# Optimization experiments

Hardware: AMD Instinct MI355X
Metric: run time of the kernel (lower is better)

Reference implementation:

```python
import jax, jax.numpy as jnp
import numpy as np
import math

B, S, D, H, L, V = 16, 512, 1024, 16, 128, 32000
DH = D // H


def _posenc(s, d):
    pos = np.arange(s, dtype=np.float32)[:, None]
    div = np.exp(np.arange(0, d, 2, dtype=np.float32) * (-math.log(10000.0) / d))
    pe = np.zeros((s, d), dtype=np.float32)
    pe[:, 0::2] = np.sin(pos * div)
    pe[:, 1::2] = np.cos(pos * div)
    return jnp.asarray(pe)


def _ln(x, g, b):
    m = jnp.mean(x, axis=-1, keepdims=True)
    v = jnp.mean((x - m) ** 2, axis=-1, keepdims=True)
    return (x - m) / jnp.sqrt(v + 1e-5) * g + b


def setup_inputs():
    key = jax.random.key(0)
    ks = jax.random.split(key, 16)
    w = lambda k, *sh: 0.02 * jax.random.normal(k, sh, dtype=jnp.float32)
    return {
        'x': jax.random.randint(ks[0], (B, S), 0, V),
        'embed': w(ks[1], V, D),
        'Wq': w(ks[2], D, D), 'bq': jnp.zeros((D,), jnp.float32),
        'Wk': w(ks[3], D, D), 'bk': jnp.zeros((D,), jnp.float32),
        'Wv': w(ks[4], D, D), 'bv': jnp.zeros((D,), jnp.float32),
        'Wo': w(ks[5], D, D), 'bo': jnp.zeros((D,), jnp.float32),
        'g1': jnp.ones((D,), jnp.float32), 'be1': jnp.zeros((D,), jnp.float32),
        'W1': w(ks[6], D, D), 'bf1': jnp.zeros((D,), jnp.float32),
        'W2': w(ks[7], D, D), 'bf2': jnp.zeros((D,), jnp.float32),
        'g2': jnp.ones((D,), jnp.float32), 'be2': jnp.zeros((D,), jnp.float32),
        'g3': jnp.ones((D,), jnp.float32), 'be3': jnp.zeros((D,), jnp.float32),
        'Wmu': w(ks[8], D, L), 'bmu': jnp.zeros((L,), jnp.float32),
        'Wsig': w(ks[9], D, L), 'bsig': jnp.zeros((L,), jnp.float32),
        'eps': jax.random.normal(ks[10], (B, S, L), dtype=jnp.float32),
    }


def reference(x, embed, Wq, bq, Wk, bk, Wv, bv, Wo, bo, g1, be1, W1, bf1, W2, bf2,
              g2, be2, g3, be3, Wmu, bmu, Wsig, bsig, eps):
    h = embed[x] * jnp.asarray(D ** 0.5, jnp.float32)          # [B,S,D]
    h = h + _posenc(S, D)                                       # dropout = identity (eval)
    h = _ln(h, g1, be1)
    # attention (faithful to source: raw reshape head-split, scale = dh/2)
    Q = (h @ Wq + bq).reshape(B, H, S, DH)
    K = (h @ Wk + bk).reshape(B, H, S, DH)
    Vv = (h @ Wv + bv).reshape(B, H, S, DH)
    scores = jnp.einsum('bhqd,bhkd->bhqk', Q, K) / (DH / 2.0)
    attn = jax.nn.softmax(scores, axis=-1)
    ctx = jnp.einsum('bhqk,bhkd->bhqd', attn, Vv).reshape(B, S, D)
    ctx = ctx @ Wo + bo
    h = h + ctx
    h = _ln(h, g2, be2)
    f = jax.nn.leaky_relu(h @ W1 + bf1, 0.01) @ W2 + bf2
    h = f + f                                                    # source: x = ffn(x); x = x + drop2(x)
    h = _ln(h, g3, be3)
    mu = h @ Wmu + bmu
    sigma = jnp.exp(h @ Wsig + bsig)
    z = mu + sigma * eps
    return z
```

## Files before the change

### kernel.cpp

```cpp
#include <hip/hip_runtime.h>
#include <cstdint>


typedef __bf16 bf16;
typedef __bf16 bf16x8 __attribute__((ext_vector_type(8)));
typedef __bf16 bf16x4 __attribute__((ext_vector_type(4)));
typedef float f32x4 __attribute__((ext_vector_type(4)));

#define MFMA16(a, b, c) __builtin_amdgcn_mfma_f32_16x16x32_bf16((a), (b), (c), 0, 0, 0)

#if __has_builtin(__builtin_amdgcn_exp2f)
#define EXP2F(x) __builtin_amdgcn_exp2f(x)
#else
#define EXP2F(x) exp2f(x)
#endif

__device__ __forceinline__ void async16(const bf16* g, bf16* l) {
  __builtin_amdgcn_global_load_lds(
      (const __attribute__((address_space(1))) unsigned int*)g,
      (__attribute__((address_space(3))) unsigned int*)l, 16, 0, 0);
}

struct TP8 {
  const float* src[8];
  bf16* dst[8];
  int ncol[8];
};
__global__ __launch_bounds__(256) void transpose8_kernel(TP8 p) {
  const int z = blockIdx.z;
  const int N = p.ncol[z];
  const int tk = blockIdx.x * 64, tn = blockIdx.y * 64;
  if (tn >= N) return;
  const float* __restrict__ W = p.src[z];
  bf16* __restrict__ Wt = p.dst[z];
  __shared__ float tile[64][65];
  const int a = threadIdx.x >> 6, b = threadIdx.x & 63;
#pragma unroll
  for (int i = 0; i < 16; ++i) {
    int k = a + i * 4;
    tile[k][b] = W[(size_t)(tk + k) * N + tn + b];
  }
  __syncthreads();
#pragma unroll
  for (int i = 0; i < 16; ++i) {
    int n = a + i * 4;
    Wt[(size_t)(tn + n) * 1024 + tk + b] = (bf16)tile[b][n];
  }
}

__global__ __launch_bounds__(256) void embed_ln_kernel(const int* __restrict__ x,
                                                       const float* __restrict__ emb,
                                                       const float* __restrict__ g,
                                                       const float* __restrict__ be,
                                                       bf16* __restrict__ obf) {
  const int w = threadIdx.x >> 6, lane = threadIdx.x & 63;
  const int row = blockIdx.x * 4 + w;
  const int s = row & 511;
  const int t = x[row];
  const int c0 = lane * 16;
  const float* er = emb + (size_t)t * 1024 + c0;
  float o[16];
#pragma unroll
  for (int i = 0; i < 4; ++i) {
    const float4 e = *(const float4*)(er + i * 4);
    o[i * 4 + 0] = e.x; o[i * 4 + 1] = e.y; o[i * 4 + 2] = e.z; o[i * 4 + 3] = e.w;
  }
#pragma unroll
  for (int p = 0; p < 8; ++p) {
    const int cc = c0 + 2 * p;
    const float freq = __expf((float)cc * (-9.210340371976184f / 1024.0f));
    const float ang = (float)s * freq;
    o[2 * p] = o[2 * p] * 32.0f + __sinf(ang);
    o[2 * p + 1] = o[2 * p + 1] * 32.0f + __cosf(ang);
  }
  float sm = 0.f, q = 0.f;
#pragma unroll
  for (int j = 0; j < 16; ++j) { sm += o[j]; q += o[j] * o[j]; }
#pragma unroll
  for (int off = 1; off < 64; off <<= 1) {
    sm += __shfl_xor(sm, off);
    q += __shfl_xor(q, off);
  }
  const float mean = sm * (1.0f / 1024.0f);
  const float var = q * (1.0f / 1024.0f) - mean * mean;
  const float rstd = rsqrtf(var + 1e-5f);
  bf16 ob[16];
#pragma unroll
  for (int i = 0; i < 4; ++i) {
    const float4 gv = *(const float4*)(g + c0 + i * 4);
    const float4 bv = *(const float4*)(be + c0 + i * 4);
    const float gvv[4] = {gv.x, gv.y, gv.z, gv.w};
    const float bvv[4] = {bv.x, bv.y, bv.z, bv.w};
#pragma unroll
    for (int j = 0; j < 4; ++j)
      ob[i * 4 + j] = (bf16)((o[i * 4 + j] - mean) * rstd * gvv[j] + bvv[j]);
  }
  bf16* dst = obf + (size_t)row * 1024 + c0;
  *(uint4*)dst = *(const uint4*)&ob[0];
  *(uint4*)(dst + 8) = *(const uint4*)&ob[8];
}

__global__ __launch_bounds__(256) void ln_kernel(const bf16* __restrict__ in,
                                                 const float* __restrict__ g,
                                                 const float* __restrict__ be,
                                                 bf16* __restrict__ obf) {
  const int w = threadIdx.x >> 6, lane = threadIdx.x & 63;
  const int row = blockIdx.x * 4 + w;
  const int c0 = lane * 16;
  const bf16* src = in + (size_t)row * 1024 + c0;
  const bf16x8 v0 = *(const bf16x8*)src;
  const bf16x8 v1 = *(const bf16x8*)(src + 8);
  float v[16];
#pragma unroll
  for (int j = 0; j < 8; ++j) { v[j] = (float)v0[j]; v[8 + j] = (float)v1[j]; }
  float s = 0.f, q = 0.f;
#pragma unroll
  for (int j = 0; j < 16; ++j) { s += v[j]; q += v[j] * v[j]; }
#pragma unroll
  for (int off = 1; off < 64; off <<= 1) {
    s += __shfl_xor(s, off);
    q += __shfl_xor(q, off);
  }
  const float mean = s * (1.0f / 1024.0f);
  const float var = q * (1.0f / 1024.0f) - mean * mean;
  const float rstd = rsqrtf(var + 1e-5f);
  bf16 ob[16];
#pragma unroll
  for (int i = 0; i < 4; ++i) {
    const float4 gv = *(const float4*)(g + c0 + i * 4);
    const float4 bv = *(const float4*)(be + c0 + i * 4);
    const float gvv[4] = {gv.x, gv.y, gv.z, gv.w};
    const float bvv[4] = {bv.x, bv.y, bv.z, bv.w};
#pragma unroll
    for (int j = 0; j < 4; ++j)
      ob[i * 4 + j] = (bf16)((v[i * 4 + j] - mean) * rstd * gvv[j] + bvv[j]);
  }
  bf16* dst = obf + (size_t)row * 1024 + c0;
  *(uint4*)dst = *(const uint4*)&ob[0];
  *(uint4*)(dst + 8) = *(const uint4*)&ob[8];
}

template <int MODE, int BK>
__global__ __launch_bounds__(256) void gemm_kernel(
    const bf16* __restrict__ A, const bf16* __restrict__ Bt,
    const float* __restrict__ b0f, const float* __restrict__ b1f,
    const float* __restrict__ b2f,
    bf16* __restrict__ o0, bf16* __restrict__ o1, bf16* __restrict__ o2,
    const bf16* __restrict__ residb,
    int M, int N, int K) {
  __shared__ __attribute__((aligned(16))) bf16 Asm[2][128 * BK];
  __shared__ __attribute__((aligned(16))) bf16 Bsm[2][128 * BK];
  constexpr int KH = BK / 32;
  constexpr int SPT = (128 * BK / 8) / 256;
  const int tid = threadIdx.x;
  const int wv = tid >> 6, lane = tid & 63;
  const int quad = lane >> 4, l15 = lane & 15;
  const int m0 = blockIdx.x * 128, n0 = blockIdx.y * 128;
  const int wm = wv & 1, wn = wv >> 1;

  f32x4 acc[4][4];
#pragma unroll
  for (int i = 0; i < 4; ++i)
#pragma unroll
    for (int j = 0; j < 4; ++j) acc[i][j] = {0.f, 0.f, 0.f, 0.f};

  const bf16* Aglb[SPT];
  const bf16* Bglb[SPT];
  int soff[SPT];
#pragma unroll
  for (int i = 0; i < SPT; ++i) {
    const int s = tid + i * 256;
    int row, col;
    if constexpr (BK == 32) {
      row = s >> 2;
      col = (s & 3) ^ ((row >> 1) & 3);
    } else {
      row = s >> 3;
      col = (s & 7) ^ (row & 7);
    }
    Aglb[i] = A + (size_t)(m0 + row) * K + col * 8;
    Bglb[i] = Bt + (size_t)(n0 + row) * K + col * 8;
    soff[i] = s * 8;
  }

#pragma unroll
  for (int i = 0; i < SPT; ++i) async16(Aglb[i], &Asm[0][soff[i]]);
#pragma unroll
  for (int i = 0; i < SPT; ++i) async16(Bglb[i], &Bsm[0][soff[i]]);
  __syncthreads();

  const int nk = K / BK;
  for (int k = 0; k < nk; ++k) {
    const int cur = k & 1, nxt = cur ^ 1;
    bf16x8 af[4][KH], bfr[4][KH];
#pragma unroll
    for (int mi = 0; mi < 4; ++mi) {
      const int row = wm * 64 + mi * 16 + l15;
#pragma unroll
      for (int h = 0; h < KH; ++h) {
        int pos;
        if constexpr (BK == 32) pos = quad ^ ((row >> 1) & 3);
        else pos = (h * 4 + quad) ^ (row & 7);
        af[mi][h] = *(const bf16x8*)(&Asm[cur][(row * (BK / 8) + pos) * 8]);
      }
    }
#pragma unroll
    for (int ni = 0; ni < 4; ++ni) {
      const int row = wn * 64 + ni * 16 + l15;
#pragma unroll
      for (int h = 0; h < KH; ++h) {
        int pos;
        if constexpr (BK == 32) pos = quad ^ ((row >> 1) & 3);
        else pos = (h * 4 + quad) ^ (row & 7);
        bfr[ni][h] = *(const bf16x8*)(&Bsm[cur][(row * (BK / 8) + pos) * 8]);
      }
    }
    if (k + 1 < nk) {
      const int ko = (k + 1) * BK;
#pragma unroll
      for (int i = 0; i < SPT; ++i) async16(Aglb[i] + ko, &Asm[nxt][soff[i]]);
#pragma unroll
      for (int i = 0; i < SPT; ++i) async16(Bglb[i] + ko, &Bsm[nxt][soff[i]]);
    }
#pragma unroll
    for (int h = 0; h < KH; ++h)
#pragma unroll
      for (int mi = 0; mi < 4; ++mi)
#pragma unroll
        for (int ni = 0; ni < 4; ++ni)
          acc[mi][ni] = MFMA16(af[mi][h], bfr[ni][h], acc[mi][ni]);
    __syncthreads();
  }

  const int part = (MODE == 6) ? (blockIdx.y >> 3) : 0;
  bf16* ob = o0;
  const float* bp = b0f;
  if constexpr (MODE == 6) {
    ob = (part == 0) ? o0 : (part == 1 ? o1 : o2);
    bp = (part == 0) ? b0f : (part == 1 ? b1f : b2f);
  }
#pragma unroll
  for (int ni = 0; ni < 4; ++ni) {
    const int col = n0 + wn * 64 + ni * 16 + l15;
    const int cl = (MODE == 6) ? (col - part * 1024) : col;
    const float bv = bp[cl];
#pragma unroll
    for (int mi = 0; mi < 4; ++mi) {
#pragma unroll
      for (int r = 0; r < 4; ++r) {
        const int row = m0 + wm * 64 + mi * 16 + quad * 4 + r;
        float v = acc[mi][ni][r] + bv;
        if constexpr (MODE == 1) {
          const size_t idx = (size_t)row * N + col;
          o0[idx] = (bf16)(v + (float)residb[idx]);
        } else if constexpr (MODE == 2) {
          o0[(size_t)row * N + col] = (bf16)(v > 0.f ? v : 0.01f * v);
        } else if constexpr (MODE == 3) {
          o0[(size_t)row * N + col] = (bf16)(2.0f * v);
        } else {
          ob[(size_t)row * 1024 + cl] = (bf16)v;
        }
      }
    }
  }
}

__global__ __launch_bounds__(256) void gemm_musig(const bf16* __restrict__ A,
                                                  const bf16* __restrict__ Bt,
                                                  const float* __restrict__ bmu,
                                                  const float* __restrict__ bsig,
                                                  float* __restrict__ of) {
  constexpr int BK = 64;
  __shared__ __attribute__((aligned(16))) bf16 Asm[2][64 * BK];
  __shared__ __attribute__((aligned(16))) bf16 Bsm[2][128 * BK];
  const int tid = threadIdx.x;
  const int wv = tid >> 6, lane = tid & 63;
  const int quad = lane >> 4, l15 = lane & 15;
  const int m0 = blockIdx.x * 64, n0 = blockIdx.y * 128;
  const int wm = wv & 1, wn = wv >> 1;

  f32x4 acc[2][4];
#pragma unroll
  for (int i = 0; i < 2; ++i)
#pragma unroll
    for (int j = 0; j < 4; ++j) acc[i][j] = {0.f, 0.f, 0.f, 0.f};

  const bf16* Aglb[2];
  int asoff[2];
#pragma unroll
  for (int i = 0; i < 2; ++i) {
    const int s = tid + i * 256;
    const int row = s >> 3, col = (s & 7) ^ (row & 7);
    Aglb[i] = A + (size_t)(m0 + row) * 1024 + col * 8;
    asoff[i] = s * 8;
  }
  const bf16* Bglb[4];
  int bsoff[4];
#pragma unroll
  for (int i = 0; i < 4; ++i) {
    const int s = tid + i * 256;
    const int row = s >> 3, col = (s & 7) ^ (row & 7);
    Bglb[i] = Bt + (size_t)(n0 + row) * 1024 + col * 8;
    bsoff[i] = s * 8;
  }

#pragma unroll
  for (int i = 0; i < 2; ++i) async16(Aglb[i], &Asm[0][asoff[i]]);
#pragma unroll
  for (int i = 0; i < 4; ++i) async16(Bglb[i], &Bsm[0][bsoff[i]]);
  __syncthreads();

  for (int k = 0; k < 16; ++k) {
    const int cur = k & 1, nxt = cur ^ 1;
    bf16x8 af[2][2], bfr[4][2];
#pragma unroll
    for (int mi = 0; mi < 2; ++mi) {
      const int row = wm * 32 + mi * 16 + l15;
#pragma unroll
      for (int h = 0; h < 2; ++h) {
        const int pos = (h * 4 + quad) ^ (row & 7);
        af[mi][h] = *(const bf16x8*)(&Asm[cur][(row * 8 + pos) * 8]);
      }
    }
#pragma unroll
    for (int ni = 0; ni < 4; ++ni) {
      const int row = wn * 64 + ni * 16 + l15;
#pragma unroll
      for (int h = 0; h < 2; ++h) {
        const int pos = (h * 4 + quad) ^ (row & 7);
        bfr[ni][h] = *(const bf16x8*)(&Bsm[cur][(row * 8 + pos) * 8]);
      }
    }
    if (k + 1 < 16) {
      const int ko = (k + 1) * BK;
#pragma unroll
      for (int i = 0; i < 2; ++i) async16(Aglb[i] + ko, &Asm[nxt][asoff[i]]);
#pragma unroll
      for (int i = 0; i < 4; ++i) async16(Bglb[i] + ko, &Bsm[nxt][bsoff[i]]);
    }
#pragma unroll
    for (int h = 0; h < 2; ++h)
#pragma unroll
      for (int mi = 0; mi < 2; ++mi)
#pragma unroll
        for (int ni = 0; ni < 4; ++ni)
          acc[mi][ni] = MFMA16(af[mi][h], bfr[ni][h], acc[mi][ni]);
    __syncthreads();
  }

#pragma unroll
  for (int ni = 0; ni < 4; ++ni) {
    const int col = n0 + wn * 64 + ni * 16 + l15;
    const float bv = (col < 128) ? bmu[col] : bsig[col - 128];
#pragma unroll
    for (int mi = 0; mi < 2; ++mi) {
#pragma unroll
      for (int r = 0; r < 4; ++r) {
        const int row = m0 + wm * 32 + mi * 16 + quad * 4 + r;
        of[(size_t)row * 256 + col] = acc[mi][ni][r] + bv;
      }
    }
  }
}

__global__ __launch_bounds__(256) void vtrans_kernel(const bf16* __restrict__ Vb,
                                                     bf16* __restrict__ VtG) {
  __shared__ float t[64][65];
  const int bh = blockIdx.x, kt = blockIdx.y;
  const int tid = threadIdx.x;
  const bf16* src = Vb + (size_t)bh * 32768 + (size_t)kt * 4096;
#pragma unroll
  for (int i = 0; i < 2; ++i) {
    int s = i * 256 + tid;
    int r = s >> 3, c = (s & 7) * 8;
    bf16x8 v = *(const bf16x8*)(src + (size_t)s * 8);
#pragma unroll
    for (int j = 0; j < 8; ++j) t[r][c + j] = (float)v[j];
  }
  __syncthreads();
  bf16* dst = VtG + (size_t)bh * 32768 + kt * 64;
#pragma unroll
  for (int i = 0; i < 2; ++i) {
    int s = i * 256 + tid;
    int d = s >> 3, kc = (s & 7) * 8;
    bf16 tmp[8];
#pragma unroll
    for (int j = 0; j < 8; ++j) tmp[j] = (bf16)t[kc + j][d];
    *(uint4*)(dst + (size_t)d * 512 + kc) = *(const uint4*)tmp;
  }
}

__global__ __launch_bounds__(256) void attn_kernel(const bf16* __restrict__ Qg,
                                                   const bf16* __restrict__ Kg,
                                                   const bf16* __restrict__ Vt,
                                                   bf16* __restrict__ ctx) {
  __shared__ __attribute__((aligned(16))) bf16 Ksm[128 * 64];
  __shared__ __attribute__((aligned(16))) bf16 Vsm[64 * 128];
  __shared__ __attribute__((aligned(16))) bf16 Psm[4][16 * 128];
  const int tid = threadIdx.x;
  const int w = tid >> 6, lane = tid & 63;
  const int quad = lane >> 4, l15 = lane & 15;
  const int bh = blockIdx.x;
  const size_t base = (size_t)bh * 32768;
  const bf16* Vth = Vt + base;
  const int qbase = blockIdx.y * 128 + w * 32;
  const f32x4 fz = {0.f, 0.f, 0.f, 0.f};

  bf16x8 a[2][2];
#pragma unroll
  for (int qt = 0; qt < 2; ++qt)
#pragma unroll
    for (int hf = 0; hf < 2; ++hf) {
      bf16x8 tq = *(const bf16x8*)(Qg + base +
                   (size_t)(qbase + qt * 16 + l15) * 64 + hf * 32 + quad * 8);
#pragma unroll
      for (int e = 0; e < 8; ++e) tq[e] = (bf16)((float)tq[e] * 0.045111758f);
      a[qt][hf] = tq;
    }

  f32x4 o[2][4];
  float l_i[2][4];
#pragma unroll
  for (int qt = 0; qt < 2; ++qt)
#pragma unroll
    for (int i = 0; i < 4; ++i) { o[qt][i] = fz; l_i[qt][i] = 0.f; }

  for (int kv0 = 0; kv0 < 512; kv0 += 128) {
#pragma unroll
    for (int i = 0; i < 4; ++i) {
      int s = i * 256 + tid;
      int r = s >> 3, c = (s & 7) ^ (r & 7);
      async16(Kg + base + (size_t)(kv0 + r) * 64 + c * 8, &Ksm[s * 8]);
    }
#pragma unroll
    for (int i = 0; i < 4; ++i) {
      int s = i * 256 + tid;
      int d = s >> 4, cs = s & 15;
      int c = (cs & 8) | ((cs & 7) ^ (d & 7));
      async16(Vth + (size_t)d * 512 + kv0 + c * 8, &Vsm[s * 8]);
    }
    __syncthreads();

    f32x4 sc[2][8];
#pragma unroll
    for (int j = 0; j < 8; ++j) {
      const int n = j * 16 + l15;
      const bf16x8 k0 = *(const bf16x8*)(&Ksm[(n * 8 + (quad ^ (n & 7))) * 8]);
      const bf16x8 k1 = *(const bf16x8*)(&Ksm[(n * 8 + ((4 + quad) ^ (n & 7))) * 8]);
      sc[0][j] = MFMA16(a[0][0], k0, fz);
      sc[0][j] = MFMA16(a[0][1], k1, sc[0][j]);
      sc[1][j] = MFMA16(a[1][0], k0, fz);
      sc[1][j] = MFMA16(a[1][1], k1, sc[1][j]);
    }

    bf16* ps = &Psm[w][0];
#pragma unroll
    for (int qt = 0; qt < 2; ++qt) {
#pragma unroll
      for (int r = 0; r < 4; ++r) {
        const int prow = quad * 4 + r;
        float sum = 0.f;
#pragma unroll
        for (int j = 0; j < 8; ++j) {
          const float p = EXP2F(sc[qt][j][r]);
          sum += p;
          const int col = j * 16 + l15;
          const int cc = col >> 3;
          const int ccs = (cc & 8) | ((cc & 7) ^ (prow & 7));
          ps[prow * 128 + ccs * 8 + (col & 7)] = (bf16)p;
        }
        l_i[qt][r] += sum;
      }
#pragma unroll
      for (int c32 = 0; c32 < 4; ++c32) {
        const int pc = c32 * 4 + quad;
        const int pcs = (pc & 8) | ((pc & 7) ^ (l15 & 7));
        const bf16x8 pf = *(const bf16x8*)(ps + l15 * 128 + pcs * 8);
#pragma unroll
        for (int ni = 0; ni < 4; ++ni) {
          const int d = ni * 16 + l15;
          const int vcs = (pc & 8) | ((pc & 7) ^ (d & 7));
          const bf16x8 vf = *(const bf16x8*)(&Vsm[(d * 16 + vcs) * 8]);
          o[qt][ni] = MFMA16(pf, vf, o[qt][ni]);
        }
      }
    }
    __syncthreads();
  }

#pragma unroll
  for (int qt = 0; qt < 2; ++qt) {
#pragma unroll
    for (int r = 0; r < 4; ++r) {
      float l = l_i[qt][r];
      l += __shfl_xor(l, 1);
      l += __shfl_xor(l, 2);
      l += __shfl_xor(l, 4);
      l += __shfl_xor(l, 8);
      const float inv = 1.0f / l;
#pragma unroll
      for (int ni = 0; ni < 4; ++ni)
        ctx[base + (size_t)(qbase + qt * 16 + quad * 4 + r) * 64 + ni * 16 + l15]
            = (bf16)(o[qt][ni][r] * inv);
    }
  }
}

__global__ __launch_bounds__(256) void final_kernel(const float* __restrict__ musg,
                                                    const float* __restrict__ eps,
                                                    float* __restrict__ z) {
  const int i = blockIdx.x * 256 + threadIdx.x;
  const int row = i >> 5;
  const int c = (i & 31) * 4;
  const float4 m = *(const float4*)(musg + (size_t)row * 256 + c);
  const float4 s = *(const float4*)(musg + (size_t)row * 256 + 128 + c);
  const float4 e = *(const float4*)(eps + (size_t)row * 128 + c);
  float4 r;
  r.x = m.x + __expf(s.x) * e.x;
  r.y = m.y + __expf(s.y) * e.y;
  r.z = m.z + __expf(s.z) * e.z;
  r.w = m.w + __expf(s.w) * e.w;
  *(float4*)(z + (size_t)row * 128 + c) = r;
}

extern "C" void kernel_launch(void* const* d_in, const int* in_sizes, int n_in,
                              void* d_out, int out_size, void* d_ws, size_t ws_size,
                              hipStream_t stream) {
  (void)in_sizes; (void)n_in; (void)out_size; (void)ws_size;
  const int* x = (const int*)d_in[0];
  const float* emb = (const float*)d_in[1];
  const float* Wq = (const float*)d_in[2];
  const float* bq = (const float*)d_in[3];
  const float* Wk = (const float*)d_in[4];
  const float* bkb = (const float*)d_in[5];
  const float* Wv = (const float*)d_in[6];
  const float* bv = (const float*)d_in[7];
  const float* Wo = (const float*)d_in[8];
  const float* bo = (const float*)d_in[9];
  const float* g1 = (const float*)d_in[10];
  const float* be1 = (const float*)d_in[11];
  const float* W1 = (const float*)d_in[12];
  const float* bf1 = (const float*)d_in[13];
  const float* W2 = (const float*)d_in[14];
  const float* bf2 = (const float*)d_in[15];
  const float* g2 = (const float*)d_in[16];
  const float* be2 = (const float*)d_in[17];
  const float* g3 = (const float*)d_in[18];
  const float* be3 = (const float*)d_in[19];
  const float* Wmu = (const float*)d_in[20];
  const float* bmu = (const float*)d_in[21];
  const float* Wsig = (const float*)d_in[22];
  const float* bsig = (const float*)d_in[23];
  const float* eps = (const float*)d_in[24];
  float* z = (float*)d_out;

  const int M = 8192, D = 1024;
  char* ws = (char*)d_ws;
  size_t off = 0;
  auto alloc = [&](size_t b) {
    char* p = ws + off;
    off += (b + 255) & ~(size_t)255;
    return p;
  };
  bf16* wqkvT = (bf16*)alloc((size_t)3072 * 1024 * 2);
  bf16* woT = (bf16*)alloc((size_t)1024 * 1024 * 2);
  bf16* w1T = (bf16*)alloc((size_t)1024 * 1024 * 2);
  bf16* w2T = (bf16*)alloc((size_t)1024 * 1024 * 2);
  bf16* wmsT = (bf16*)alloc((size_t)256 * 1024 * 2);
  bf16* hb = (bf16*)alloc((size_t)M * D * 2);
  bf16* Qb = (bf16*)alloc((size_t)M * D * 2);
  bf16* Kb = (bf16*)alloc((size_t)M * D * 2);
  bf16* Vb = (bf16*)alloc((size_t)M * D * 2);
  bf16* VtG = (bf16*)alloc((size_t)M * D * 2);
  bf16* Cb = (bf16*)alloc((size_t)M * D * 2);
  bf16* h2b = (bf16*)alloc((size_t)M * D * 2);
  bf16* h3b = (bf16*)alloc((size_t)M * D * 2);
  bf16* hidb = (bf16*)alloc((size_t)M * D * 2);
  bf16* h4b = (bf16*)alloc((size_t)M * D * 2);
  bf16* h5b = (bf16*)alloc((size_t)M * D * 2);
  float* musg = (float*)alloc((size_t)M * 256 * 4);

  dim3 b256(256);
  TP8 tp;
  tp.src[0] = Wq;   tp.dst[0] = wqkvT;                        tp.ncol[0] = 1024;
  tp.src[1] = Wk;   tp.dst[1] = wqkvT + (size_t)1024 * 1024;  tp.ncol[1] = 1024;
  tp.src[2] = Wv;   tp.dst[2] = wqkvT + (size_t)2048 * 1024;  tp.ncol[2] = 1024;
  tp.src[3] = Wo;   tp.dst[3] = woT;                          tp.ncol[3] = 1024;
  tp.src[4] = W1;   tp.dst[4] = w1T;                          tp.ncol[4] = 1024;
  tp.src[5] = W2;   tp.dst[5] = w2T;                          tp.ncol[5] = 1024;
  tp.src[6] = Wmu;  tp.dst[6] = wmsT;                         tp.ncol[6] = 128;
  tp.src[7] = Wsig; tp.dst[7] = wmsT + (size_t)128 * 1024;    tp.ncol[7] = 128;
  transpose8_kernel<<<dim3(16, 16, 8), b256, 0, stream>>>(tp);

  embed_ln_kernel<<<2048, b256, 0, stream>>>(x, emb, g1, be1, hb);

  gemm_kernel<6, 32><<<dim3(64, 24), b256, 0, stream>>>(hb, wqkvT, bq, bkb, bv,
                                                        Qb, Kb, Vb, nullptr,
                                                        M, 3072, D);
  vtrans_kernel<<<dim3(256, 8), b256, 0, stream>>>(Vb, VtG);
  attn_kernel<<<dim3(256, 4), b256, 0, stream>>>(Qb, Kb, VtG, Cb);

  gemm_kernel<1, 64><<<dim3(64, 8), b256, 0, stream>>>(Cb, woT, bo, nullptr, nullptr,
                                                       h2b, nullptr, nullptr, hb,
                                                       M, D, D);
  ln_kernel<<<2048, b256, 0, stream>>>(h2b, g2, be2, h3b);
  gemm_kernel<2, 64><<<dim3(64, 8), b256, 0, stream>>>(h3b, w1T, bf1, nullptr, nullptr,
                                                       hidb, nullptr, nullptr, nullptr,
                                                       M, D, D);
  gemm_kernel<3, 64><<<dim3(64, 8), b256, 0, stream>>>(hidb, w2T, bf2, nullptr, nullptr,
                                                       h4b, nullptr, nullptr, nullptr,
                                                       M, D, D);
  ln_kernel<<<2048, b256, 0, stream>>>(h4b, g3, be3, h5b);
  gemm_musig<<<dim3(128, 2), b256, 0, stream>>>(h5b, wmsT, bmu, bsig, musg);
  final_kernel<<<1024, b256, 0, stream>>>(musg, eps, z);
}
```

Baseline: 444.6 us.

## Replace GEMM with 8-wave 128x256 tile ping-pong pipelined kernel

Replaces the 4-wave 128x128 GEMM with an 8-wave kernel that computes a 128x256 tile. The K loop is split into barrier-separated phases that interleave LDS fragment loads, async global-to-LDS staging and MFMA groups, using explicit vmcnt waits and raised MFMA priority. The aim is to overlap memory traffic with matrix math and to reuse the A tile across a wider N. In exchange the grid is smaller (fewer blocks per GEMM), there are many more barriers, and the hand-placed waits must exactly match the outstanding loads.

```diff
diff --git a/kernel.cpp b/kernel.cpp
--- a/kernel.cpp
+++ b/kernel.cpp
@@ -20,6 +20,13 @@
       (const __attribute__((address_space(1))) unsigned int*)g,
       (__attribute__((address_space(3))) unsigned int*)l, 16, 0, 0);
 }
+
+#define VMWAIT(N)                                        \
+  do {                                                   \
+    asm volatile("s_waitcnt vmcnt(" #N ")" ::: "memory"); \
+    __builtin_amdgcn_sched_barrier(0);                   \
+  } while (0)
+#define BAR() __builtin_amdgcn_s_barrier()
 
 struct TP8 {
   const float* src[8];
@@ -140,23 +147,51 @@
   *(uint4*)(dst + 8) = *(const uint4*)&ob[8];
 }
 
-template <int MODE, int BK>
-__global__ __launch_bounds__(256) void gemm_kernel(
+__device__ __forceinline__ void ld_frags2(const bf16* sm, int rbase, int l15,
+                                          int quad, bf16x8 out[2][2]) {
+#pragma unroll
+  for (int f = 0; f < 2; ++f) {
+    const int row = rbase + f * 16 + l15;
+    const int rx = row & 7;
+#pragma unroll
+    for (int h = 0; h < 2; ++h) {
+      const int c = (h * 4 + quad) ^ rx;
+      out[f][h] = *(const bf16x8*)(sm + (row * 8 + c) * 8);
+    }
+  }
+}
+
+template <int MQ, int NQ>
+__device__ __forceinline__ void mma8(const bf16x8 aF[2][2], const bf16x8 bF[2][2],
+                                     f32x4 acc[4][4]) {
+  __builtin_amdgcn_s_setprio(1);
+#pragma unroll
+  for (int h = 0; h < 2; ++h)
+#pragma unroll
+    for (int m2 = 0; m2 < 2; ++m2)
+#pragma unroll
+      for (int n2 = 0; n2 < 2; ++n2)
+        acc[MQ * 2 + m2][NQ * 2 + n2] =
+            MFMA16(aF[m2][h], bF[n2][h], acc[MQ * 2 + m2][NQ * 2 + n2]);
+  __builtin_amdgcn_s_setprio(0);
+}
+
+template <int MODE>
+__global__ __launch_bounds__(512, 2) void gemm8_kernel(
     const bf16* __restrict__ A, const bf16* __restrict__ Bt,
     const float* __restrict__ b0f, const float* __restrict__ b1f,
     const float* __restrict__ b2f,
     bf16* __restrict__ o0, bf16* __restrict__ o1, bf16* __restrict__ o2,
     const bf16* __restrict__ residb,
     int M, int N, int K) {
-  __shared__ __attribute__((aligned(16))) bf16 Asm[2][128 * BK];
-  __shared__ __attribute__((aligned(16))) bf16 Bsm[2][128 * BK];
-  constexpr int KH = BK / 32;
-  constexpr int SPT = (128 * BK / 8) / 256;
+  (void)M;
+  __shared__ __attribute__((aligned(16))) bf16 Asm[2][128 * 64];
+  __shared__ __attribute__((aligned(16))) bf16 Bsm[2][256 * 64];
   const int tid = threadIdx.x;
   const int wv = tid >> 6, lane = tid & 63;
   const int quad = lane >> 4, l15 = lane & 15;
-  const int m0 = blockIdx.x * 128, n0 = blockIdx.y * 128;
   const int wm = wv & 1, wn = wv >> 1;
+  const int m0 = blockIdx.x * 128, n0 = blockIdx.y * 256;
 
   f32x4 acc[4][4];
 #pragma unroll
@@ -164,75 +199,83 @@
 #pragma unroll
     for (int j = 0; j < 4; ++j) acc[i][j] = {0.f, 0.f, 0.f, 0.f};
 
-  const bf16* Aglb[SPT];
-  const bf16* Bglb[SPT];
-  int soff[SPT];
-#pragma unroll
-  for (int i = 0; i < SPT; ++i) {
-    const int s = tid + i * 256;
-    int row, col;
-    if constexpr (BK == 32) {
-      row = s >> 2;
-      col = (s & 3) ^ ((row >> 1) & 3);
-    } else {
-      row = s >> 3;
-      col = (s & 7) ^ (row & 7);
-    }
-    Aglb[i] = A + (size_t)(m0 + row) * K + col * 8;
-    Bglb[i] = Bt + (size_t)(n0 + row) * K + col * 8;
-    soff[i] = s * 8;
-  }
-
-#pragma unroll
-  for (int i = 0; i < SPT; ++i) async16(Aglb[i], &Asm[0][soff[i]]);
-#pragma unroll
-  for (int i = 0; i < SPT; ++i) async16(Bglb[i], &Bsm[0][soff[i]]);
-  __syncthreads();
-
-  const int nk = K / BK;
-  for (int k = 0; k < nk; ++k) {
-    const int cur = k & 1, nxt = cur ^ 1;
-    bf16x8 af[4][KH], bfr[4][KH];
-#pragma unroll
-    for (int mi = 0; mi < 4; ++mi) {
-      const int row = wm * 64 + mi * 16 + l15;
-#pragma unroll
-      for (int h = 0; h < KH; ++h) {
-        int pos;
-        if constexpr (BK == 32) pos = quad ^ ((row >> 1) & 3);
-        else pos = (h * 4 + quad) ^ (row & 7);
-        af[mi][h] = *(const bf16x8*)(&Asm[cur][(row * (BK / 8) + pos) * 8]);
-      }
-    }
-#pragma unroll
-    for (int ni = 0; ni < 4; ++ni) {
-      const int row = wn * 64 + ni * 16 + l15;
-#pragma unroll
-      for (int h = 0; h < KH; ++h) {
-        int pos;
-        if constexpr (BK == 32) pos = quad ^ ((row >> 1) & 3);
-        else pos = (h * 4 + quad) ^ (row & 7);
-        bfr[ni][h] = *(const bf16x8*)(&Bsm[cur][(row * (BK / 8) + pos) * 8]);
-      }
-    }
-    if (k + 1 < nk) {
-      const int ko = (k + 1) * BK;
-#pragma unroll
-      for (int i = 0; i < SPT; ++i) async16(Aglb[i] + ko, &Asm[nxt][soff[i]]);
-#pragma unroll
-      for (int i = 0; i < SPT; ++i) async16(Bglb[i] + ko, &Bsm[nxt][soff[i]]);
-    }
-#pragma unroll
-    for (int h = 0; h < KH; ++h)
-#pragma unroll
-      for (int mi = 0; mi < 4; ++mi)
-#pragma unroll
-        for (int ni = 0; ni < 4; ++ni)
-          acc[mi][ni] = MFMA16(af[mi][h], bfr[ni][h], acc[mi][ni]);
-    __syncthreads();
-  }
-
-  const int part = (MODE == 6) ? (blockIdx.y >> 3) : 0;
+  size_t aoff[2], boff[2];
+  int slds[2];
+#pragma unroll
+  for (int i = 0; i < 2; ++i) {
+    const int s = tid + i * 512;
+    const int r = s >> 3, c = (s & 7) ^ (r & 7);
+    aoff[i] = (size_t)(m0 + r) * K + c * 8;
+    boff[i] = (size_t)(n0 + r) * K + c * 8;
+    slds[i] = s * 8;
+  }
+  auto stageA = [&](int buf, int t) {
+#pragma unroll
+    for (int i = 0; i < 2; ++i) async16(A + aoff[i] + t * 64, &Asm[buf][slds[i]]);
+  };
+  auto stageB = [&](int buf, int hh, int t) {
+    const size_t ho = (size_t)hh * 128 * K;
+    const int hl = hh * 8192;
+#pragma unroll
+    for (int i = 0; i < 2; ++i)
+      async16(Bt + boff[i] + ho + t * 64, &Bsm[buf][hl + slds[i]]);
+  };
+
+  stageB(0, 0, 0); stageB(0, 1, 0); stageA(0, 0);
+  stageB(1, 0, 1); stageB(1, 1, 1); stageA(1, 1);
+  VMWAIT(6);
+  BAR();
+
+  bf16x8 aF[2][2], bF0[2][2], bF1[2][2];
+  const int am0 = wm * 64, bn0 = wn * 64;
+
+  auto phases = [&](int ne, int no, bool hn) {
+    ld_frags2(&Asm[0][0], am0, l15, quad, aF);
+    ld_frags2(&Bsm[0][0], bn0, l15, quad, bF0);
+    BAR();
+    mma8<0, 0>(aF, bF0, acc);
+    BAR();
+    ld_frags2(&Bsm[0][0], bn0 + 32, l15, quad, bF1);
+    BAR();
+    mma8<0, 1>(aF, bF1, acc);
+    BAR();
+    ld_frags2(&Asm[0][0], am0 + 32, l15, quad, aF);
+    if (hn) stageB(0, 0, ne);
+    BAR();
+    mma8<1, 1>(aF, bF1, acc);
+    BAR();
+    if (hn) stageB(0, 1, ne);
+    BAR();
+    mma8<1, 0>(aF, bF0, acc);
+    if (hn) { VMWAIT(4); } else { VMWAIT(0); }
+    BAR();
+    ld_frags2(&Asm[1][0], am0, l15, quad, aF);
+    ld_frags2(&Bsm[1][0], bn0, l15, quad, bF0);
+    if (hn) stageA(0, ne);
+    BAR();
+    mma8<0, 0>(aF, bF0, acc);
+    BAR();
+    ld_frags2(&Bsm[1][0], bn0 + 32, l15, quad, bF1);
+    BAR();
+    mma8<0, 1>(aF, bF1, acc);
+    BAR();
+    ld_frags2(&Asm[1][0], am0 + 32, l15, quad, aF);
+    if (hn) stageB(1, 0, no);
+    BAR();
+    mma8<1, 1>(aF, bF1, acc);
+    BAR();
+    if (hn) { stageB(1, 1, no); stageA(1, no); }
+    BAR();
+    mma8<1, 0>(aF, bF0, acc);
+    if (hn) { VMWAIT(6); }
+    BAR();
+  };
+
+  const int nIter = K >> 7;
+  for (int it = 0; it + 1 < nIter; ++it) phases(2 * it + 2, 2 * it + 3, true);
+  phases(0, 0, false);
+
+  const int part = (MODE == 6) ? ((int)blockIdx.y >> 2) : 0;
   bf16* ob = o0;
   const float* bp = b0f;
   if constexpr (MODE == 6) {
@@ -581,6 +624,7 @@
   float* musg = (float*)alloc((size_t)M * 256 * 4);
 
   dim3 b256(256);
+  dim3 b512(512);
   TP8 tp;
   tp.src[0] = Wq;   tp.dst[0] = wqkvT;                        tp.ncol[0] = 1024;
   tp.src[1] = Wk;   tp.dst[1] = wqkvT + (size_t)1024 * 1024;  tp.ncol[1] = 1024;
@@ -594,22 +638,22 @@
 
   embed_ln_kernel<<<2048, b256, 0, stream>>>(x, emb, g1, be1, hb);
 
-  gemm_kernel<6, 32><<<dim3(64, 24), b256, 0, stream>>>(hb, wqkvT, bq, bkb, bv,
-                                                        Qb, Kb, Vb, nullptr,
-                                                        M, 3072, D);
+  gemm8_kernel<6><<<dim3(64, 12), b512, 0, stream>>>(hb, wqkvT, bq, bkb, bv,
+                                                     Qb, Kb, Vb, nullptr,
+                                                     M, 3072, D);
   vtrans_kernel<<<dim3(256, 8), b256, 0, stream>>>(Vb, VtG);
   attn_kernel<<<dim3(256, 4), b256, 0, stream>>>(Qb, Kb, VtG, Cb);
 
-  gemm_kernel<1, 64><<<dim3(64, 8), b256, 0, stream>>>(Cb, woT, bo, nullptr, nullptr,
-                                                       h2b, nullptr, nullptr, hb,
-                                                       M, D, D);
+  gemm8_kernel<1><<<dim3(64, 4), b512, 0, stream>>>(Cb, woT, bo, nullptr, nullptr,
+                                                    h2b, nullptr, nullptr, hb,
+                                                    M, D, D);
   ln_kernel<<<2048, b256, 0, stream>>>(h2b, g2, be2, h3b);
-  gemm_kernel<2, 64><<<dim3(64, 8), b256, 0, stream>>>(h3b, w1T, bf1, nullptr, nullptr,
-                                                       hidb, nullptr, nullptr, nullptr,
-                                                       M, D, D);
-  gemm_kernel<3, 64><<<dim3(64, 8), b256, 0, stream>>>(hidb, w2T, bf2, nullptr, nullptr,
-                                                       h4b, nullptr, nullptr, nullptr,
-                                                       M, D, D);
+  gemm8_kernel<2><<<dim3(64, 4), b512, 0, stream>>>(h3b, w1T, bf1, nullptr, nullptr,
+                                                    hidb, nullptr, nullptr, nullptr,
+                                                    M, D, D);
+  gemm8_kernel<3><<<dim3(64, 4), b512, 0, stream>>>(hidb, w2T, bf2, nullptr, nullptr,
+                                                    h4b, nullptr, nullptr, nullptr,
+                                                    M, D, D);
   ln_kernel<<<2048, b256, 0, stream>>>(h4b, g3, be3, h5b);
   gemm_musig<<<dim3(128, 2), b256, 0, stream>>>(h5b, wmsT, bmu, bsig, musg);
   final_kernel<<<1024, b256, 0, stream>>>(musg, eps, z);
```

Measured after the change: 438.1 us. Within noise of the previous version (-1.5%).
